# Kernel optimization log

Measured on AMD Instinct MI355X. Metric: run time of the kernel, lower is better.

## Reference

```python
import jax, jax.numpy as jnp
import numpy as np
import math

B, S, P, G = 8, 512, 64, 64
E, GE = 768, 32          # sub_embed_dim, gene_embed_dim
HD = E // 2              # sub_head_dim = 384
L = P * G
LAMBDA_INIT = 0.8 - 0.6 * math.exp(-0.3 * 0)  # depth=0 -> 0.2
SCALING = HD ** -0.5


def setup_inputs() -> dict:
    key0 = jax.random.key(0)
    ks = jax.random.split(key0, 12)
    init = 0.02
    return {
        "query": jax.random.normal(ks[0], (B, S, E), jnp.float32),
        "key": jax.random.normal(ks[1], (B, P, G, GE), jnp.float32),
        "query_mask": jax.random.bernoulli(ks[2], 0.9, (B, S)),
        "key_mask": jax.random.bernoulli(ks[3], 0.9, (B, P, G)),
        # weights stored [in, out] so y = x @ W (equiv to torch Linear no-bias)
        "Wq": jax.random.normal(ks[4], (E, E), jnp.float32) * init,
        "Wkv": jax.random.normal(ks[5], (GE, 2 * E), jnp.float32) * init,
        "Wout": jax.random.normal(ks[6], (E, E), jnp.float32) * init,
        "lambda_q1": jax.random.normal(ks[7], (HD,), jnp.float32) * 0.1,
        "lambda_k1": jax.random.normal(ks[8], (HD,), jnp.float32) * 0.1,
        "lambda_q2": jax.random.normal(ks[9], (HD,), jnp.float32) * 0.1,
        "lambda_k2": jax.random.normal(ks[10], (HD,), jnp.float32) * 0.1,
        "ln_weight": jnp.ones((E,), jnp.float32),  # RMSNorm affine weight (2*HD = E)
    }


def reference(query, key, query_mask, key_mask, Wq, Wkv, Wout,
              lambda_q1, lambda_k1, lambda_q2, lambda_k2, ln_weight):
    # Projections
    Q = query @ Wq                                   # [B,S,E]
    KV = key.reshape(B, L, GE) @ Wkv                 # [B,L,2E]
    K = KV[..., :E]                                  # [B,L,E]
    V = KV[..., E:]                                  # [B,L,E] (= 2*HD)

    # Split into 2 heads of dim HD
    Qh = Q.reshape(B, S, 2, HD).transpose(0, 2, 1, 3) * SCALING   # [B,2,S,HD]
    Kh = K.reshape(B, L, 2, HD).transpose(0, 2, 1, 3)             # [B,2,L,HD]

    # Combined mask [B,S,L]
    mask = query_mask[:, :, None] & key_mask.reshape(B, L)[:, None, :]

    # Dual attention scores + stable softmax (eps=1e-8 on denominator)
    scores = jnp.einsum('bhsd,bhld->bhsl', Qh, Kh)                # [B,2,S,L]
    scores = jnp.where(mask[:, None], scores, -1e20)
    m = jnp.max(scores, axis=-1, keepdims=True)
    p = jnp.exp(scores - m)
    attn = p / (jnp.sum(p, axis=-1, keepdims=True) + 1e-8)

    # Differential combination
    lam = (jnp.exp(jnp.sum(lambda_q1 * lambda_k1))
           - jnp.exp(jnp.sum(lambda_q2 * lambda_k2)) + LAMBDA_INIT)
    diff = attn[:, 0] - lam * attn[:, 1]                          # [B,S,L]
    diff = diff - jnp.min(diff, axis=-1, keepdims=True) + 1e-20
    diff = jnp.where(mask, diff, 0.0)

    # Value contraction: [B,S,L] @ [B,L,E] -> [B,S,E]
    attn_out = jnp.einsum('bsl,ble->bse', diff, V)

    # RMSNorm (eps=1e-5, affine) then scale by (1 - lambda_init)
    ms = jnp.mean(attn_out * attn_out, axis=-1, keepdims=True)
    attn_out = attn_out * jax.lax.rsqrt(ms + 1e-5) * ln_weight
    attn_out = attn_out * (1.0 - LAMBDA_INIT)

    out = attn_out @ Wout                                         # [B,S,E]
    return out, diff.reshape(B, S, P, G)
```

## Files before the change

### kernel.cpp

```cpp
#include <hip/hip_runtime.h>
#include <math.h>

#define LAM_INIT 0.2f
#define ONE_MINUS_LAM 0.8f
#define SCALING_F 0.05103103630798288f

__device__ inline float waveMax(float v) {
#pragma unroll
    for (int o = 32; o > 0; o >>= 1) v = fmaxf(v, __shfl_xor(v, o));
    return v;
}
__device__ inline float waveMin(float v) {
#pragma unroll
    for (int o = 32; o > 0; o >>= 1) v = fminf(v, __shfl_xor(v, o));
    return v;
}
__device__ inline float waveSum(float v) {
#pragma unroll
    for (int o = 32; o > 0; o >>= 1) v += __shfl_xor(v, o);
    return v;
}

__global__ __launch_bounds__(256) void k01_prep(
    const float* __restrict__ key, const float* __restrict__ Wq,
    const float* __restrict__ Wkv, const float* __restrict__ Wout,
    const float* __restrict__ lq1, const float* __restrict__ lk1,
    const float* __restrict__ lq2, const float* __restrict__ lk2,
    const float* __restrict__ ln,
    float* __restrict__ keyT, float* __restrict__ Wcomb,
    float* __restrict__ Wvp, float* __restrict__ lam)
{
    int blk = blockIdx.x;
    int tid = threadIdx.x;
    if (blk < 128) {
        int b  = blk >> 4;
        int l0 = (blk & 15) << 8;
        __shared__ float tile[256 * 33];
        const float* kp = key + ((size_t)b * 4096 + l0) * 32;
#pragma unroll
        for (int q = 0; q < 32; ++q) {
            int idx = tid + (q << 8);
            int r = idx >> 5, g = idx & 31;
            tile[r * 33 + g] = kp[idx];
        }
        __syncthreads();
        float* op = keyT + (size_t)b * 32 * 4096 + l0;
#pragma unroll
        for (int q = 0; q < 32; ++q) {
            int idx = tid + (q << 8);
            int g = idx >> 8, ll = idx & 255;
            op[(size_t)g * 4096 + ll] = tile[ll * 33 + g];
        }
    } else if (blk < 512) {
        int bb = blk - 128;
        int kc = bb & 1;
        int ob = bb >> 1;
        int idx = ob * 256 + tid;
        int e  = idx >> 6;
        int hg = idx & 63;
        int h = hg >> 5, g = hg & 31;
        const float4* wqr = (const float4*)(Wq  + (size_t)e * 768 + h * 384 + kc * 192);
        const float4* wkr = (const float4*)(Wkv + (size_t)g * 1536 + h * 384 + kc * 192);
        float s0 = 0.f, s1 = 0.f;
#pragma unroll 4
        for (int d = 0; d < 48; d += 2) {
            float4 a0 = wqr[d],   b0 = wkr[d];
            float4 a1 = wqr[d+1], b1 = wkr[d+1];
            s0 += a0.x*b0.x + a0.y*b0.y + a0.z*b0.z + a0.w*b0.w;
            s1 += a1.x*b1.x + a1.y*b1.y + a1.z*b1.z + a1.w*b1.w;
        }
        atomicAdd(&Wcomb[idx], (s0 + s1) * SCALING_F);
    } else if (blk < 1280) {
        int bb = blk - 512;
        int kc = bb / 96;
        int ob = bb - kc * 96;
        int idx = ob * 256 + tid;
        int g = idx / 768;
        int e = idx - g * 768;
        const float* wvr = Wkv + (size_t)g * 1536 + 768;
        int c0 = kc * 96;
        float s0 = 0.f, s1 = 0.f;
#pragma unroll 4
        for (int c = c0; c < c0 + 96; c += 2) {
            s0 += wvr[c]   * ln[c]   * Wout[(size_t)c * 768 + e];
            s1 += wvr[c+1] * ln[c+1] * Wout[(size_t)(c+1) * 768 + e];
        }
        Wvp[kc * 24576 + idx] = s0 + s1;
    } else {
        float s1 = 0.f, s2 = 0.f;
        for (int d = tid; d < 384; d += 256) {
            s1 += lq1[d] * lk1[d];
            s2 += lq2[d] * lk2[d];
        }
        s1 = waveSum(s1);
        s2 = waveSum(s2);
        __shared__ float r1[4], r2[4];
        int wid = tid >> 6, lane = tid & 63;
        if (lane == 0) { r1[wid] = s1; r2[wid] = s2; }
        __syncthreads();
        if (tid == 0) {
            float a  = r1[0] + r1[1] + r1[2] + r1[3];
            float b2 = r2[0] + r2[1] + r2[2] + r2[3];
            lam[0] = expf(a) - expf(b2) + LAM_INIT;
        }
    }
}

__global__ __launch_bounds__(256) void k2_qt(
    const float* __restrict__ query, const float* __restrict__ Wcomb,
    const float* __restrict__ Wvp, float* __restrict__ Wvo,
    float* __restrict__ Qt)
{
    int blk = blockIdx.x;
    int tid = threadIdx.x;
    if (blk >= 256) {
        int idx = (blk - 256) * 256 + tid;
        float s = 0.f;
#pragma unroll
        for (int kc = 0; kc < 8; ++kc) s += Wvp[kc * 24576 + idx];
        Wvo[idx] = s;
        return;
    }
    int m0 = blk * 16;
    __shared__ __align__(16) float Aq[16 * 772];
#pragma unroll
    for (int q = 0; q < 12; ++q) {
        int f = tid + q * 256;
        int r = f / 192, c4 = f - r * 192;
        float4 v = *(const float4*)&query[(size_t)(m0 + r) * 768 + c4 * 4];
        *(float4*)&Aq[r * 772 + c4 * 4] = v;
    }
    __syncthreads();

    int n0 = (tid & 15) * 4;
    int ml = tid >> 4;
    const float* arow = &Aq[ml * 772];
    float ax = 0.f, ay = 0.f, az = 0.f, aw = 0.f;
    for (int k = 0; k < 768; k += 8) {
#pragma unroll
        for (int j = 0; j < 8; ++j) {
            float a = arow[k + j];
            float4 w = *(const float4*)&Wcomb[(size_t)(k + j) * 64 + n0];
            ax += a * w.x; ay += a * w.y; az += a * w.z; aw += a * w.w;
        }
    }
    float4 o; o.x = ax; o.y = ay; o.z = az; o.w = aw;
    *(float4*)&Qt[(size_t)(m0 + ml) * 64 + n0] = o;
}

__global__ __launch_bounds__(512, 4) void k3_attn(
    const float* __restrict__ Qt, const float* __restrict__ keyT,
    const int* __restrict__ qmask, const int* __restrict__ kmask,
    const float* __restrict__ lamp, float* __restrict__ diffO)
{
    int blk = blockIdx.x;
    int b  = blk >> 7;
    int s0 = (blk & 127) * 4;
    int tid = threadIdx.x;
    int lane = tid & 63, wid = tid >> 6;

    __shared__ __align__(16) float qt_t[32 * 8];
    __shared__ float red[64];

    if (tid < 256) {
        int ts = tid >> 6, c2 = tid & 63;
        int h = c2 >> 5, g = c2 & 31;
        qt_t[g * 8 + (ts << 1) + h] = Qt[(size_t)(b * 512 + s0 + ts) * 64 + c2];
    }
    int qm[4];
#pragma unroll
    for (int ts = 0; ts < 4; ++ts) qm[ts] = qmask[b * 512 + s0 + ts];
    float lam = lamp[0];

    unsigned kmb = 0;
#pragma unroll
    for (int c = 0; c < 2; ++c) {
        int4 km = *(const int4*)(kmask + b * 4096 + c * 2048 + tid * 4);
        if (km.x) kmb |= 1u << (c * 4 + 0);
        if (km.y) kmb |= 1u << (c * 4 + 1);
        if (km.z) kmb |= 1u << (c * 4 + 2);
        if (km.w) kmb |= 1u << (c * 4 + 3);
    }
    __syncthreads();

    float p[2][4][8];
#pragma unroll
    for (int h = 0; h < 2; ++h)
#pragma unroll
        for (int ts = 0; ts < 4; ++ts)
#pragma unroll
            for (int i = 0; i < 8; ++i) p[h][ts][i] = 0.f;

    const float* kt = keyT + (size_t)b * 131072 + tid * 4;
    for (int g = 0; g < 32; ++g) {
        float qv[8];
        *(float4*)&qv[0] = *(const float4*)&qt_t[g * 8];
        *(float4*)&qv[4] = *(const float4*)&qt_t[g * 8 + 4];
        const float* kg = kt + (size_t)g * 4096;
#pragma unroll
        for (int c = 0; c < 2; ++c) {
            float4 kv = *(const float4*)(kg + c * 2048);
#pragma unroll
            for (int ts = 0; ts < 4; ++ts)
#pragma unroll
                for (int h = 0; h < 2; ++h) {
                    float q = qv[ts * 2 + h];
                    p[h][ts][c*4+0] += q * kv.x;
                    p[h][ts][c*4+1] += q * kv.y;
                    p[h][ts][c*4+2] += q * kv.z;
                    p[h][ts][c*4+3] += q * kv.w;
                }
        }
    }

#pragma unroll
    for (int h = 0; h < 2; ++h)
#pragma unroll
        for (int ts = 0; ts < 4; ++ts)
#pragma unroll
            for (int i = 0; i < 8; ++i) {
                bool ok = qm[ts] && ((kmb >> i) & 1u);
                p[h][ts][i] = ok ? p[h][ts][i] : -1e20f;
            }

    float mrow[2][4];
#pragma unroll
    for (int h = 0; h < 2; ++h)
#pragma unroll
        for (int ts = 0; ts < 4; ++ts) {
            float v = -3.4e38f;
#pragma unroll
            for (int i = 0; i < 8; ++i) v = fmaxf(v, p[h][ts][i]);
            v = waveMax(v);
            if (lane == 0) red[(h * 4 + ts) * 8 + wid] = v;
        }
    __syncthreads();
#pragma unroll
    for (int h = 0; h < 2; ++h)
#pragma unroll
        for (int ts = 0; ts < 4; ++ts) {
            int r = (h * 4 + ts) * 8;
            float v = red[r];
#pragma unroll
            for (int w = 1; w < 8; ++w) v = fmaxf(v, red[r + w]);
            mrow[h][ts] = v;
        }
    __syncthreads();

    float inv[2][4];
#pragma unroll
    for (int h = 0; h < 2; ++h)
#pragma unroll
        for (int ts = 0; ts < 4; ++ts) {
            float s = 0.f;
#pragma unroll
            for (int i = 0; i < 8; ++i) {
                float e2 = __expf(p[h][ts][i] - mrow[h][ts]);
                p[h][ts][i] = e2;
                s += e2;
            }
            s = waveSum(s);
            if (lane == 0) red[(h * 4 + ts) * 8 + wid] = s;
        }
    __syncthreads();
#pragma unroll
    for (int h = 0; h < 2; ++h)
#pragma unroll
        for (int ts = 0; ts < 4; ++ts) {
            int r = (h * 4 + ts) * 8;
            float s = red[r];
#pragma unroll
            for (int w = 1; w < 8; ++w) s += red[r + w];
            inv[h][ts] = 1.0f / (s + 1e-8f);
        }
    __syncthreads();

    float mn[4];
#pragma unroll
    for (int ts = 0; ts < 4; ++ts) {
        float v = 3.4e38f;
#pragma unroll
        for (int i = 0; i < 8; ++i) {
            float d = p[0][ts][i] * inv[0][ts] - lam * (p[1][ts][i] * inv[1][ts]);
            p[0][ts][i] = d;
            v = fminf(v, d);
        }
        v = waveMin(v);
        if (lane == 0) red[ts * 8 + wid] = v;
    }
    __syncthreads();
#pragma unroll
    for (int ts = 0; ts < 4; ++ts) {
        int r = ts * 8;
        float v = red[r];
#pragma unroll
        for (int w = 1; w < 8; ++w) v = fminf(v, red[r + w]);
        mn[ts] = v;
    }

#pragma unroll
    for (int ts = 0; ts < 4; ++ts) {
        size_t base = (size_t)(b * 512 + s0 + ts) * 4096 + tid * 4;
#pragma unroll
        for (int c = 0; c < 2; ++c) {
            float4 o;
            float v0 = p[0][ts][c*4+0] - mn[ts] + 1e-20f;
            float v1 = p[0][ts][c*4+1] - mn[ts] + 1e-20f;
            float v2 = p[0][ts][c*4+2] - mn[ts] + 1e-20f;
            float v3 = p[0][ts][c*4+3] - mn[ts] + 1e-20f;
            o.x = (qm[ts] && ((kmb >> (c*4+0)) & 1u)) ? v0 : 0.f;
            o.y = (qm[ts] && ((kmb >> (c*4+1)) & 1u)) ? v1 : 0.f;
            o.z = (qm[ts] && ((kmb >> (c*4+2)) & 1u)) ? v2 : 0.f;
            o.w = (qm[ts] && ((kmb >> (c*4+3)) & 1u)) ? v3 : 0.f;
            *(float4*)(diffO + base + c * 2048) = o;
        }
    }
}

__global__ __launch_bounds__(256) void k4_T(
    const float* __restrict__ diff, const float* __restrict__ key,
    float* __restrict__ P)
{
    int blk = blockIdx.x;
    int rt = blk & 31, kc = blk >> 5;
    int row0 = rt << 7;
    int b = row0 >> 9;
    int l0 = kc << 9;
    int tid = threadIdx.x;
    int tx = tid & 7;
    int ty = tid >> 3;
    int g0 = tx * 4;

    __shared__ __align__(16) float Ks[256][32];

    float acc[4][4];
#pragma unroll
    for (int r = 0; r < 4; ++r)
#pragma unroll
        for (int c2 = 0; c2 < 4; ++c2) acc[r][c2] = 0.f;

    for (int ph = 0; ph < 2; ++ph) {
        int lp = l0 + ph * 256;
        __syncthreads();
#pragma unroll
        for (int q = 0; q < 32; ++q) {
            int idx = tid + (q << 8);
            int r = idx >> 5, g = idx & 31;
            Ks[r][g] = key[((size_t)(b * 4096 + lp + r)) * 32 + g];
        }
        __syncthreads();

        for (int j4 = 0; j4 < 64; ++j4) {
            int l = lp + j4 * 4;
            float4 dv[4];
#pragma unroll
            for (int r = 0; r < 4; ++r)
                dv[r] = *(const float4*)(diff + (size_t)(row0 + ty * 4 + r) * 4096 + l);
#pragma unroll
            for (int jj = 0; jj < 4; ++jj) {
                float4 kq = *(const float4*)&Ks[j4 * 4 + jj][g0];
#pragma unroll
                for (int r = 0; r < 4; ++r) {
                    float d = (jj == 0) ? dv[r].x : (jj == 1) ? dv[r].y : (jj == 2) ? dv[r].z : dv[r].w;
                    acc[r][0] += d * kq.x;
                    acc[r][1] += d * kq.y;
                    acc[r][2] += d * kq.z;
                    acc[r][3] += d * kq.w;
                }
            }
        }
    }
#pragma unroll
    for (int r = 0; r < 4; ++r) {
        float4 o; o.x = acc[r][0]; o.y = acc[r][1]; o.z = acc[r][2]; o.w = acc[r][3];
        *(float4*)&P[(size_t)kc * 131072 + (size_t)(row0 + ty * 4 + r) * 32 + g0] = o;
    }
}

__global__ __launch_bounds__(256) void k5_out(
    const float* __restrict__ P, const float* __restrict__ Wkv,
    const float* __restrict__ Wvo, float* __restrict__ out)
{
    int row0 = blockIdx.x * 8;
    int tid = threadIdx.x;
    int wid = tid >> 6, lane = tid & 63;
    __shared__ __align__(16) float Ts[8][32];
    __shared__ float red[8][4];
    __shared__ float rs_s[8];

    {
        int r = tid >> 5, g = tid & 31;
        float s = 0.f;
#pragma unroll
        for (int kc = 0; kc < 8; ++kc)
            s += P[(size_t)kc * 131072 + (size_t)(row0 + r) * 32 + g];
        Ts[r][g] = s;
    }
    __syncthreads();

    float ssq[8];
#pragma unroll
    for (int r = 0; r < 8; ++r) ssq[r] = 0.f;

#pragma unroll
    for (int ec = 0; ec < 3; ++ec) {
        int e = tid + ec * 256;
        float wv[32];
#pragma unroll
        for (int g = 0; g < 32; ++g) wv[g] = Wkv[(size_t)g * 1536 + 768 + e];
#pragma unroll
        for (int r = 0; r < 8; ++r) {
            float a = 0.f;
#pragma unroll
            for (int g = 0; g < 32; ++g) a += Ts[r][g] * wv[g];
            ssq[r] += a * a;
        }
    }
#pragma unroll
    for (int r = 0; r < 8; ++r) {
        float v = waveSum(ssq[r]);
        if (lane == 0) red[r][wid] = v;
    }
    __syncthreads();
    if (tid < 8) {
        float s = red[tid][0] + red[tid][1] + red[tid][2] + red[tid][3];
        float ms = s * (1.0f / 768.0f);
        rs_s[tid] = rsqrtf(ms + 1e-5f) * ONE_MINUS_LAM;
    }
    __syncthreads();

#pragma unroll
    for (int ec = 0; ec < 3; ++ec) {
        int e = tid + ec * 256;
        float wo[32];
#pragma unroll
        for (int g = 0; g < 32; ++g) wo[g] = Wvo[(size_t)g * 768 + e];
#pragma unroll
        for (int r = 0; r < 8; ++r) {
            float o = 0.f;
#pragma unroll
            for (int g = 0; g < 32; ++g) o += Ts[r][g] * wo[g];
            out[(size_t)(row0 + r) * 768 + e] = o * rs_s[r];
        }
    }
}

extern "C" void kernel_launch(void* const* d_in, const int* in_sizes, int n_in,
                              void* d_out, int out_size, void* d_ws, size_t ws_size,
                              hipStream_t stream) {
    (void)in_sizes; (void)n_in; (void)out_size; (void)ws_size;
    const float* query = (const float*)d_in[0];
    const float* key   = (const float*)d_in[1];
    const int*   qmask = (const int*)d_in[2];
    const int*   kmask = (const int*)d_in[3];
    const float* Wq    = (const float*)d_in[4];
    const float* Wkv   = (const float*)d_in[5];
    const float* Wout  = (const float*)d_in[6];
    const float* lq1   = (const float*)d_in[7];
    const float* lk1   = (const float*)d_in[8];
    const float* lq2   = (const float*)d_in[9];
    const float* lk2   = (const float*)d_in[10];
    const float* ln    = (const float*)d_in[11];

    float* out  = (float*)d_out;
    float* diff = out + 3145728;

    float* ws    = (float*)d_ws;
    float* Wcomb = ws;
    float* Wvo   = ws + 49152;
    float* Wvp   = ws + 73728;
    float* lam   = ws + 270336;
    float* Qt    = ws + 270400;
    float* keyT  = ws + 532544;
    float* P     = ws + 1581120;

    hipMemsetAsync(Wcomb, 0, 49152 * sizeof(float), stream);
    k01_prep<<<1281, 256, 0, stream>>>(key, Wq, Wkv, Wout, lq1, lk1, lq2, lk2, ln,
                                       keyT, Wcomb, Wvp, lam);
    k2_qt<<<352, 256, 0, stream>>>(query, Wcomb, Wvp, Wvo, Qt);
    k3_attn<<<1024, 512, 0, stream>>>(Qt, keyT, qmask, kmask, lam, diff);
    k4_T<<<256, 256, 0, stream>>>(diff, key, P);
    k5_out<<<512, 256, 0, stream>>>(P, Wkv, Wvo, out);
}
```

Before: 269.3 us.

## Use fp16 packed keys with fdot2 scores, split-K Qt GEMM, drop memset

The transposed key is now stored as packed fp16 pairs, and the score loop in the attention kernel uses packed dot2 instructions. This halves key traffic and FMA count, at the cost of fp16 rounding error in the softmax inputs. Wcomb atomics and the memset are replaced by two partial buffers that are summed when loaded. The Qt projection becomes a split-K tiled GEMM whose four partials are summed in the attention kernel, and k4 uses smaller row tiles so it launches twice as many blocks. P reuses the Qtp workspace.

```diff
diff --git a/kernel.cpp b/kernel.cpp
--- a/kernel.cpp
+++ b/kernel.cpp
@@ -4,6 +4,17 @@
 #define LAM_INIT 0.2f
 #define ONE_MINUS_LAM 0.8f
 #define SCALING_F 0.05103103630798288f
+
+typedef _Float16 h2 __attribute__((ext_vector_type(2)));
+
+#if defined(__has_builtin)
+#if __has_builtin(__builtin_amdgcn_fdot2)
+#define FDOT2(a, b, c) __builtin_amdgcn_fdot2((a), (b), (c), false)
+#endif
+#endif
+#ifndef FDOT2
+#define FDOT2(a, b, c) ((float)(a).x * (float)(b).x + ((float)(a).y * (float)(b).y + (c)))
+#endif
 
 __device__ inline float waveMax(float v) {
 #pragma unroll
@@ -27,7 +38,7 @@
     const float* __restrict__ lq1, const float* __restrict__ lk1,
     const float* __restrict__ lq2, const float* __restrict__ lk2,
     const float* __restrict__ ln,
-    float* __restrict__ keyT, float* __restrict__ Wcomb,
+    unsigned* __restrict__ keyThU, float* __restrict__ Wcp,
     float* __restrict__ Wvp, float* __restrict__ lam)
 {
     int blk = blockIdx.x;
@@ -44,12 +55,13 @@
             tile[r * 33 + g] = kp[idx];
         }
         __syncthreads();
-        float* op = keyT + (size_t)b * 32 * 4096 + l0;
-#pragma unroll
-        for (int q = 0; q < 32; ++q) {
-            int idx = tid + (q << 8);
-            int g = idx >> 8, ll = idx & 255;
-            op[(size_t)g * 4096 + ll] = tile[ll * 33 + g];
+#pragma unroll
+        for (int gp = 0; gp < 16; ++gp) {
+            h2 v;
+            v.x = (_Float16)tile[tid * 33 + 2 * gp];
+            v.y = (_Float16)tile[tid * 33 + 2 * gp + 1];
+            keyThU[((size_t)(b * 16 + gp)) * 4096 + l0 + tid] =
+                __builtin_bit_cast(unsigned, v);
         }
     } else if (blk < 512) {
         int bb = blk - 128;
@@ -69,7 +81,7 @@
             s0 += a0.x*b0.x + a0.y*b0.y + a0.z*b0.z + a0.w*b0.w;
             s1 += a1.x*b1.x + a1.y*b1.y + a1.z*b1.z + a1.w*b1.w;
         }
-        atomicAdd(&Wcomb[idx], (s0 + s1) * SCALING_F);
+        Wcp[kc * 49152 + idx] = (s0 + s1) * SCALING_F;
     } else if (blk < 1280) {
         int bb = blk - 512;
         int kc = bb / 96;
@@ -107,49 +119,74 @@
 }
 
 __global__ __launch_bounds__(256) void k2_qt(
-    const float* __restrict__ query, const float* __restrict__ Wcomb,
+    const float* __restrict__ query, const float* __restrict__ Wcp,
     const float* __restrict__ Wvp, float* __restrict__ Wvo,
-    float* __restrict__ Qt)
+    float* __restrict__ Qtp)
 {
     int blk = blockIdx.x;
     int tid = threadIdx.x;
-    if (blk >= 256) {
-        int idx = (blk - 256) * 256 + tid;
+    if (blk >= 512) {
+        int idx = (blk - 512) * 256 + tid;
         float s = 0.f;
 #pragma unroll
         for (int kc = 0; kc < 8; ++kc) s += Wvp[kc * 24576 + idx];
         Wvo[idx] = s;
         return;
     }
-    int m0 = blk * 16;
-    __shared__ __align__(16) float Aq[16 * 772];
-#pragma unroll
-    for (int q = 0; q < 12; ++q) {
-        int f = tid + q * 256;
-        int r = f / 192, c4 = f - r * 192;
-        float4 v = *(const float4*)&query[(size_t)(m0 + r) * 768 + c4 * 4];
-        *(float4*)&Aq[r * 772 + c4 * 4] = v;
-    }
-    __syncthreads();
-
-    int n0 = (tid & 15) * 4;
-    int ml = tid >> 4;
-    const float* arow = &Aq[ml * 772];
-    float ax = 0.f, ay = 0.f, az = 0.f, aw = 0.f;
-    for (int k = 0; k < 768; k += 8) {
-#pragma unroll
-        for (int j = 0; j < 8; ++j) {
-            float a = arow[k + j];
-            float4 w = *(const float4*)&Wcomb[(size_t)(k + j) * 64 + n0];
-            ax += a * w.x; ay += a * w.y; az += a * w.z; aw += a * w.w;
-        }
-    }
-    float4 o; o.x = ax; o.y = ay; o.z = az; o.w = aw;
-    *(float4*)&Qt[(size_t)(m0 + ml) * 64 + n0] = o;
+    int kc = blk >> 7;
+    int mt = blk & 127;
+    int m0 = mt * 32;
+    __shared__ __align__(16) float As[64 * 33];
+    __shared__ __align__(16) float Bs[64 * 64];
+
+    int tm = tid >> 5;
+    int tn = tid & 31;
+    float acc[4][2];
+#pragma unroll
+    for (int r = 0; r < 4; ++r) { acc[r][0] = 0.f; acc[r][1] = 0.f; }
+
+    for (int ch = 0; ch < 3; ++ch) {
+        int k0 = kc * 192 + ch * 64;
+        __syncthreads();
+#pragma unroll
+        for (int q = 0; q < 2; ++q) {
+            int f = tid + q * 256;
+            int m = f >> 4, kq = f & 15;
+            float4 v = *(const float4*)&query[(size_t)(m0 + m) * 768 + k0 + kq * 4];
+            As[(kq * 4 + 0) * 33 + m] = v.x;
+            As[(kq * 4 + 1) * 33 + m] = v.y;
+            As[(kq * 4 + 2) * 33 + m] = v.z;
+            As[(kq * 4 + 3) * 33 + m] = v.w;
+        }
+#pragma unroll
+        for (int q = 0; q < 4; ++q) {
+            int f = tid + q * 256;
+            int kk = f >> 4, n4 = f & 15;
+            float4 a = *(const float4*)&Wcp[(size_t)(k0 + kk) * 64 + n4 * 4];
+            float4 b = *(const float4*)&Wcp[49152 + (size_t)(k0 + kk) * 64 + n4 * 4];
+            float4 s; s.x = a.x + b.x; s.y = a.y + b.y; s.z = a.z + b.z; s.w = a.w + b.w;
+            *(float4*)&Bs[kk * 64 + n4 * 4] = s;
+        }
+        __syncthreads();
+#pragma unroll 8
+        for (int kk = 0; kk < 64; ++kk) {
+            float4 a = *(const float4*)&As[kk * 33 + tm * 4];
+            float2 b = *(const float2*)&Bs[kk * 64 + tn * 2];
+            acc[0][0] += a.x * b.x; acc[0][1] += a.x * b.y;
+            acc[1][0] += a.y * b.x; acc[1][1] += a.y * b.y;
+            acc[2][0] += a.z * b.x; acc[2][1] += a.z * b.y;
+            acc[3][0] += a.w * b.x; acc[3][1] += a.w * b.y;
+        }
+    }
+#pragma unroll
+    for (int r = 0; r < 4; ++r) {
+        float2 o; o.x = acc[r][0]; o.y = acc[r][1];
+        *(float2*)&Qtp[(size_t)kc * 262144 + (size_t)(m0 + tm * 4 + r) * 64 + tn * 2] = o;
+    }
 }
 
 __global__ __launch_bounds__(512, 4) void k3_attn(
-    const float* __restrict__ Qt, const float* __restrict__ keyT,
+    const float* __restrict__ Qtp, const unsigned* __restrict__ keyThU,
     const int* __restrict__ qmask, const int* __restrict__ kmask,
     const float* __restrict__ lamp, float* __restrict__ diffO)
 {
@@ -159,13 +196,23 @@
     int tid = threadIdx.x;
     int lane = tid & 63, wid = tid >> 6;
 
-    __shared__ __align__(16) float qt_t[32 * 8];
+    __shared__ __align__(16) unsigned qt_th[128];
     __shared__ float red[64];
 
-    if (tid < 256) {
-        int ts = tid >> 6, c2 = tid & 63;
-        int h = c2 >> 5, g = c2 & 31;
-        qt_t[g * 8 + (ts << 1) + h] = Qt[(size_t)(b * 512 + s0 + ts) * 64 + c2];
+    if (tid < 128) {
+        int ts = tid >> 5;
+        int h  = (tid >> 4) & 1;
+        int gp = tid & 15;
+        size_t row = (size_t)(b * 512 + s0 + ts) * 64;
+        int col = h * 32 + 2 * gp;
+        float v0 = 0.f, v1 = 0.f;
+#pragma unroll
+        for (int kc = 0; kc < 4; ++kc) {
+            v0 += Qtp[(size_t)kc * 262144 + row + col];
+            v1 += Qtp[(size_t)kc * 262144 + row + col + 1];
+        }
+        h2 hv; hv.x = (_Float16)v0; hv.y = (_Float16)v1;
+        qt_th[gp * 8 + ts * 2 + h] = __builtin_bit_cast(unsigned, hv);
     }
     int qm[4];
 #pragma unroll
@@ -191,24 +238,32 @@
 #pragma unroll
             for (int i = 0; i < 8; ++i) p[h][ts][i] = 0.f;
 
-    const float* kt = keyT + (size_t)b * 131072 + tid * 4;
-    for (int g = 0; g < 32; ++g) {
-        float qv[8];
-        *(float4*)&qv[0] = *(const float4*)&qt_t[g * 8];
-        *(float4*)&qv[4] = *(const float4*)&qt_t[g * 8 + 4];
-        const float* kg = kt + (size_t)g * 4096;
+    const unsigned* kt = keyThU + (size_t)b * 16 * 4096 + tid * 4;
+    for (int gp = 0; gp < 16; ++gp) {
+        uint4 q0 = *(const uint4*)&qt_th[gp * 8];
+        uint4 q1 = *(const uint4*)&qt_th[gp * 8 + 4];
+        h2 qv[8];
+        qv[0] = __builtin_bit_cast(h2, q0.x); qv[1] = __builtin_bit_cast(h2, q0.y);
+        qv[2] = __builtin_bit_cast(h2, q0.z); qv[3] = __builtin_bit_cast(h2, q0.w);
+        qv[4] = __builtin_bit_cast(h2, q1.x); qv[5] = __builtin_bit_cast(h2, q1.y);
+        qv[6] = __builtin_bit_cast(h2, q1.z); qv[7] = __builtin_bit_cast(h2, q1.w);
+        const unsigned* kg = kt + (size_t)gp * 4096;
 #pragma unroll
         for (int c = 0; c < 2; ++c) {
-            float4 kv = *(const float4*)(kg + c * 2048);
+            uint4 kv = *(const uint4*)(kg + c * 2048);
+            h2 k0 = __builtin_bit_cast(h2, kv.x);
+            h2 k1 = __builtin_bit_cast(h2, kv.y);
+            h2 k2 = __builtin_bit_cast(h2, kv.z);
+            h2 k3 = __builtin_bit_cast(h2, kv.w);
 #pragma unroll
             for (int ts = 0; ts < 4; ++ts)
 #pragma unroll
                 for (int h = 0; h < 2; ++h) {
-                    float q = qv[ts * 2 + h];
-                    p[h][ts][c*4+0] += q * kv.x;
-                    p[h][ts][c*4+1] += q * kv.y;
-                    p[h][ts][c*4+2] += q * kv.z;
-                    p[h][ts][c*4+3] += q * kv.w;
+                    h2 q = qv[ts * 2 + h];
+                    p[h][ts][c*4+0] = FDOT2(k0, q, p[h][ts][c*4+0]);
+                    p[h][ts][c*4+1] = FDOT2(k1, q, p[h][ts][c*4+1]);
+                    p[h][ts][c*4+2] = FDOT2(k2, q, p[h][ts][c*4+2]);
+                    p[h][ts][c*4+3] = FDOT2(k3, q, p[h][ts][c*4+3]);
                 }
         }
     }
@@ -322,8 +377,8 @@
     float* __restrict__ P)
 {
     int blk = blockIdx.x;
-    int rt = blk & 31, kc = blk >> 5;
-    int row0 = rt << 7;
+    int rt = blk & 63, kc = blk >> 6;
+    int row0 = rt << 6;
     int b = row0 >> 9;
     int l0 = kc << 9;
     int tid = threadIdx.x;
@@ -333,9 +388,9 @@
 
     __shared__ __align__(16) float Ks[256][32];
 
-    float acc[4][4];
-#pragma unroll
-    for (int r = 0; r < 4; ++r)
+    float acc[2][4];
+#pragma unroll
+    for (int r = 0; r < 2; ++r)
 #pragma unroll
         for (int c2 = 0; c2 < 4; ++c2) acc[r][c2] = 0.f;
 
@@ -352,15 +407,15 @@
 
         for (int j4 = 0; j4 < 64; ++j4) {
             int l = lp + j4 * 4;
-            float4 dv[4];
-#pragma unroll
-            for (int r = 0; r < 4; ++r)
-                dv[r] = *(const float4*)(diff + (size_t)(row0 + ty * 4 + r) * 4096 + l);
+            float4 dv[2];
+#pragma unroll
+            for (int r = 0; r < 2; ++r)
+                dv[r] = *(const float4*)(diff + (size_t)(row0 + ty * 2 + r) * 4096 + l);
 #pragma unroll
             for (int jj = 0; jj < 4; ++jj) {
                 float4 kq = *(const float4*)&Ks[j4 * 4 + jj][g0];
 #pragma unroll
-                for (int r = 0; r < 4; ++r) {
+                for (int r = 0; r < 2; ++r) {
                     float d = (jj == 0) ? dv[r].x : (jj == 1) ? dv[r].y : (jj == 2) ? dv[r].z : dv[r].w;
                     acc[r][0] += d * kq.x;
                     acc[r][1] += d * kq.y;
@@ -371,9 +426,9 @@
         }
     }
 #pragma unroll
-    for (int r = 0; r < 4; ++r) {
+    for (int r = 0; r < 2; ++r) {
         float4 o; o.x = acc[r][0]; o.y = acc[r][1]; o.z = acc[r][2]; o.w = acc[r][3];
-        *(float4*)&P[(size_t)kc * 131072 + (size_t)(row0 + ty * 4 + r) * 32 + g0] = o;
+        *(float4*)&P[(size_t)kc * 131072 + (size_t)(row0 + ty * 2 + r) * 32 + g0] = o;
     }
 }
 
@@ -465,20 +520,19 @@
     float* out  = (float*)d_out;
     float* diff = out + 3145728;
 
-    float* ws    = (float*)d_ws;
-    float* Wcomb = ws;
-    float* Wvo   = ws + 49152;
-    float* Wvp   = ws + 73728;
-    float* lam   = ws + 270336;
-    float* Qt    = ws + 270400;
-    float* keyT  = ws + 532544;
-    float* P     = ws + 1581120;
-
-    hipMemsetAsync(Wcomb, 0, 49152 * sizeof(float), stream);
+    float* ws      = (float*)d_ws;
+    float* Wcp     = ws;
+    float* Wvo     = ws + 98304;
+    float* Wvp     = ws + 122880;
+    float* lam     = ws + 319488;
+    unsigned* keyThU = (unsigned*)(ws + 319552);
+    float* Qtp     = ws + 843840;
+    float* P       = Qtp;
+
     k01_prep<<<1281, 256, 0, stream>>>(key, Wq, Wkv, Wout, lq1, lk1, lq2, lk2, ln,
-                                       keyT, Wcomb, Wvp, lam);
-    k2_qt<<<352, 256, 0, stream>>>(query, Wcomb, Wvp, Wvo, Qt);
-    k3_attn<<<1024, 512, 0, stream>>>(Qt, keyT, qmask, kmask, lam, diff);
-    k4_T<<<256, 256, 0, stream>>>(diff, key, P);
+                                       keyThU, Wcp, Wvp, lam);
+    k2_qt<<<608, 256, 0, stream>>>(query, Wcp, Wvp, Wvo, Qtp);
+    k3_attn<<<1024, 512, 0, stream>>>(Qtp, keyThU, qmask, kmask, lam, diff);
+    k4_T<<<512, 256, 0, stream>>>(diff, key, P);
     k5_out<<<512, 256, 0, stream>>>(P, Wkv, Wvo, out);
 }
```

Result: faster. 236.0 us (-12.3%).
